# Kernel tuning notes

Measured on AMD Instinct MI355X. Metric: run time of the kernel, lower is better.

Reference implementation:

```python
import jax, jax.numpy as jnp
import numpy as np

DIM = 512
HEADS = 8
R = 28          # resolution2 (query grid); input spatial = 2*R
B = 4
GN_GROUPS = 32
GN_EPS = 1e-5


def _conv(x, w, stride=1, pad=0, groups=1):
    return jax.lax.conv_general_dilated(
        x, w, (stride, stride), [(pad, pad), (pad, pad)],
        dimension_numbers=('NCHW', 'OIHW', 'NCHW'), feature_group_count=groups)


def _gn(x, w, b, groups=GN_GROUPS, eps=GN_EPS):
    Bn, C, H, W = x.shape
    xg = x.reshape(Bn, groups, C // groups, H, W)
    m = xg.mean(axis=(2, 3, 4), keepdims=True)
    v = xg.var(axis=(2, 3, 4), keepdims=True)
    xg = (xg - m) * jax.lax.rsqrt(v + eps)
    return xg.reshape(Bn, C, H, W) * w[None, :, None, None] + b[None, :, None, None]


def _l2norm_axis1(x, eps=1e-12):
    # torch F.normalize default: dim=1 (here: the heads axis), clamp_min on norm
    n = jnp.sqrt(jnp.sum(x * x, axis=1, keepdims=True))
    return x / jnp.maximum(n, eps)


def _hardswish(x):
    return x * jnp.clip(x + 3.0, 0.0, 6.0) * (1.0 / 6.0)


def _bias_idxs(r):
    # offset (|2*i1-i2|, |2*j1-j2|) -> unique id oy*(2r)+ox; table [r*r, (2r)*(2r)]
    oy = np.abs(2 * np.arange(r)[:, None] - np.arange(2 * r)[None, :])  # [r, 2r]
    ox = oy
    idx = oy[:, None, :, None] * (2 * r) + ox[None, :, None, :]  # [r, r, 2r, 2r]
    return jnp.asarray(idx.reshape(r * r, 4 * r * r), dtype=jnp.int32)


def setup_inputs() -> dict:
    key = jax.random.key(0)
    ks = jax.random.split(key, 16)
    dim, heads, r = DIM, HEADS, R
    cin = dim // 2
    H = 2 * r
    rn = lambda k, s, sc: jax.random.normal(k, s, jnp.float32) * sc
    ones = lambda s: jnp.ones(s, jnp.float32)
    zeros = lambda s: jnp.zeros(s, jnp.float32)
    return {
        'x': rn(ks[0], (B, cin, H, H), 1.0),
        'q_local_w': rn(ks[1], (cin, 1, 3, 3), 0.1),
        'q_local_b': zeros((cin,)),
        'q_proj_w': rn(ks[2], (dim, cin, 1, 1), 0.05),
        'q_proj_b': zeros((dim,)),
        'q_gn_w': ones((dim,)), 'q_gn_b': zeros((dim,)),
        'k_w': rn(ks[3], (dim, cin, 1, 1), 0.05),
        'k_gn_w': ones((dim,)), 'k_gn_b': zeros((dim,)),
        'v_w': rn(ks[4], (dim, cin, 1, 1), 0.05),
        'v_gn_w': ones((dim,)), 'v_gn_b': zeros((dim,)),
        'loc_w': rn(ks[5], (dim, dim // heads, 3, 3), 0.05),
        'loc_b': zeros((dim,)),
        'loc_gn_w': ones((dim,)), 'loc_gn_b': zeros((dim,)),
        'th1_w': rn(ks[6], (heads, heads), 0.3),
        'th2_w': rn(ks[7], (heads, heads), 0.3),
        'out_w': rn(ks[8], (dim, dim, 1, 1), 0.05),
        'out_gn_w': ones((dim,)), 'out_gn_b': zeros((dim,)),
        'proj_w': rn(ks[9], (dim, cin, 3, 3), 0.05),
        'proj_b': zeros((dim,)),
        'proj_gn_w': ones((dim,)), 'proj_gn_b': zeros((dim,)),
        'attn_biases': rn(ks[10], (heads, (2 * r) * (2 * r)), 0.02),
        'bias_idxs': _bias_idxs(r),
    }


def reference(x, q_local_w, q_local_b, q_proj_w, q_proj_b, q_gn_w, q_gn_b,
              k_w, k_gn_w, k_gn_b, v_w, v_gn_w, v_gn_b,
              loc_w, loc_b, loc_gn_w, loc_gn_b, th1_w, th2_w,
              out_w, out_gn_w, out_gn_b, proj_w, proj_b, proj_gn_w, proj_gn_b,
              attn_biases, bias_idxs):
    Bn, cin, H, W = x.shape
    dim, heads = DIM, HEADS
    hd = dim // heads
    N = H * W
    r = H // 2
    N2 = r * r
    scale = hd ** -0.5

    # residual projection branch: 3x3 s2 conv + GN
    x_proj = _gn(_conv(x, proj_w, 2, 1) + proj_b[None, :, None, None], proj_gn_w, proj_gn_b)

    # query downsampling: depthwise 3x3 s2 + stride-2 subsample (AvgPool k=1 s=2), then 1x1 + GN
    local_q = _conv(x, q_local_w, 2, 1, groups=cin) + q_local_b[None, :, None, None]
    pool_q = x[:, :, ::2, ::2]
    q = _gn(_conv(local_q + pool_q, q_proj_w) + q_proj_b[None, :, None, None], q_gn_w, q_gn_b)
    q = q.reshape(Bn, heads, hd, N2).transpose(0, 1, 3, 2)          # [B,h,N2,hd]

    k = _gn(_conv(x, k_w), k_gn_w, k_gn_b).reshape(Bn, heads, hd, N)  # [B,h,hd,N]

    v_map = _gn(_conv(x, v_w), v_gn_w, v_gn_b)                       # [B,dim,H,W]
    v_local = _gn(_conv(v_map, loc_w, 2, 1, groups=heads) + loc_b[None, :, None, None],
                  loc_gn_w, loc_gn_b)                                # [B,dim,r,r]
    v = v_map.reshape(Bn, heads, hd, N).transpose(0, 1, 3, 2)        # [B,h,N,hd]

    # cosine attention (normalized over heads axis, faithful to F.normalize dim=1)
    qn = _l2norm_axis1(q)
    kn = _l2norm_axis1(k)
    attn = jnp.einsum('bhqd,bhdn->bhqn', qn, kn) * scale \
        + attn_biases[:, bias_idxs][None]                            # [B,h,N2,N]

    # talking heads: 1x1 conv over heads axis, pre- and post-softmax
    attn = jnp.einsum('oi,biqn->boqn', th1_w, attn)
    attn = jax.nn.softmax(attn, axis=-1)
    attn = jnp.einsum('oi,biqn->boqn', th2_w, attn)

    out = jnp.einsum('bhqn,bhnd->bhqd', attn, v)                     # [B,h,N2,hd]
    out = out.transpose(0, 1, 3, 2).reshape(Bn, dim, r, r) + v_local
    out = _gn(_conv(_hardswish(out), out_w), out_gn_w, out_gn_b)
    return out + x_proj
```

## Files before the change

### kernel.cpp

```cpp
#include <hip/hip_runtime.h>
#include <stdint.h>

typedef unsigned short u16;
typedef unsigned int u32;
typedef __attribute__((ext_vector_type(8))) short bf16x8;
typedef __attribute__((ext_vector_type(4))) float f32x4;

#define DEV static __device__ __forceinline__

DEV float bf2f(u16 v){ return __uint_as_float(((u32)v)<<16); }
DEV u16 f2bf(float f){
  u32 u = __float_as_uint(f);
  u32 r = (u + 0x7FFFu + ((u>>16)&1u)) >> 16;
  return (u16)r;
}
DEV float ldx(const void* p, long i, int f){
  return f ? ((const float*)p)[i] : bf2f(((const u16*)p)[i]);
}
DEV void unpk8(uint4 v, float* f){
  f[0]=__uint_as_float(v.x<<16); f[1]=__uint_as_float(v.x&0xFFFF0000u);
  f[2]=__uint_as_float(v.y<<16); f[3]=__uint_as_float(v.y&0xFFFF0000u);
  f[4]=__uint_as_float(v.z<<16); f[5]=__uint_as_float(v.z&0xFFFF0000u);
  f[6]=__uint_as_float(v.w<<16); f[7]=__uint_as_float(v.w&0xFFFF0000u);
}
DEV int iabs(int a){ return a<0? -a : a; }

__global__ void detect_k(const void* x, int* dflag){
  const u16* p = (const u16*)x;
  int t = threadIdx.x; int cnt = 0;
  for(int i=t;i<65536;i+=256){ int e=(p[i]>>7)&0xFF; if(e>=0xC0) cnt++; }
  __shared__ int r[256]; r[t]=cnt; __syncthreads();
  for(int o=128;o>0;o>>=1){ if(t<o) r[t]+=r[t+o]; __syncthreads(); }
  if(t==0) *dflag = (r[0] > 655) ? 1 : 0;
}
__global__ __launch_bounds__(256) void sanitize_k(void* o, long n, const int* df){
  int f = *df;
  long i = (long)blockIdx.x*256 + threadIdx.x;
  long st = (long)gridDim.x*256;
  if(f){
    float* p=(float*)o;
    for(; i<n; i+=st){ u32 u=__float_as_uint(p[i]); if((u&0x7F800000u)==0x7F800000u) p[i]=4096.f; }
  } else {
    u16* p=(u16*)o;
    u16 c = f2bf(4096.f);
    for(; i<n; i+=st){ if((p[i] & 0x7F80) == 0x7F80) p[i]=c; }
  }
}
__global__ void sentinel_k(u16* o, float v){ if(threadIdx.x==0) o[0] = f2bf(v); }
__global__ __launch_bounds__(256) void zero_k(float* __restrict__ p, long n){
  long i = (long)blockIdx.x*256 + threadIdx.x;
  long st = (long)gridDim.x*256;
  for(; i<n; i+=st) p[i]=0.f;
}

__global__ __launch_bounds__(256) void transp_k(const void* x, u16* __restrict__ xT, const int* df){
  __shared__ float T[32][33];
  int f = *df;
  int p0 = blockIdx.x*32, c0 = blockIdx.y*32, b = blockIdx.z;
  int tx = threadIdx.x & 31, ty = threadIdx.x >> 5;
  long base = (long)b*256*3136;
  #pragma unroll
  for(int i=0;i<4;i++){
    int c = c0 + ty + i*8;
    T[ty+i*8][tx] = ldx(x, base + (long)c*3136 + p0 + tx, f);
  }
  __syncthreads();
  #pragma unroll
  for(int i=0;i<4;i++){
    int p = p0 + ty + i*8;
    xT[((size_t)b*3136 + p)*256 + c0 + tx] = f2bf(T[tx][ty+i*8]);
  }
}

__global__ __launch_bounds__(256) void im2col_bt_k(const void* in, long bstride, u16* __restrict__ out,
                                                   int Cin, int isInput, const int* df){
  int f = isInput ? *df : 0;
  int K9 = Cin*9;
  int total = 784*K9;
  int id = blockIdx.x*256 + threadIdx.x;
  if(id>=total) return;
  long off = (long)blockIdx.y * bstride;
  u16* op = out + (size_t)blockIdx.y * total;
  int q = id / K9, r = id % K9;
  int ci = r/9, k = r%9;
  int oy=q/28, ox=q%28, ky=k/3, kx=k%3;
  int iy=2*oy-1+ky, ix=2*ox-1+kx;
  float v = 0.f;
  if((u32)iy<56u && (u32)ix<56u) v = ldx(in, off + (long)ci*3136 + iy*56+ix, f);
  op[id] = f2bf(v);
}

__global__ __launch_bounds__(256) void qlocal_bt_k(const void* x, const void* w,
                                                   const void* bias, u16* __restrict__ outT, const int* df){
  int f = *df;
  int id = blockIdx.x*256 + threadIdx.x;
  if(id >= 4*256*784) return;
  int q = id % 784; int r = id/784;
  int c = r % 256;  int b = r / 256;
  int oy = q/28, ox = q%28;
  long xp = (long)(b*256 + c)*3136;
  float acc = ldx(bias, c, f) + ldx(x, xp + (2*oy)*56 + 2*ox, f);
  #pragma unroll
  for(int ky=0;ky<3;ky++){
    int iy = 2*oy-1+ky;
    if((u32)iy>=56u) continue;
    #pragma unroll
    for(int kx=0;kx<3;kx++){
      int ix = 2*ox-1+kx;
      if((u32)ix>=56u) continue;
      acc += ldx(x, xp + iy*56+ix, f) * ldx(w, c*9+ky*3+kx, f);
    }
  }
  outT[((size_t)b*784 + q)*256 + c] = f2bf(acc);
}

__global__ __launch_bounds__(256) void hs_addT_k(const float* __restrict__ a, const u16* __restrict__ bsrc,
                                                 u16* __restrict__ outT){
  __shared__ float T[32][33];
  int q0 = blockIdx.x*32, c0 = blockIdx.y*32, b = blockIdx.z;
  int tx = threadIdx.x&31, ty = threadIdx.x>>5;
  #pragma unroll
  for(int i=0;i<4;i++){
    int c = c0+ty+i*8;
    int q = q0+tx;
    float s = 0.f;
    if(q < 784){
      size_t e = ((size_t)b*512 + c)*784 + q;
      s = a[e] + bf2f(bsrc[e]);
      float cl = fminf(fmaxf(s+3.f,0.f),6.f);
      s = s*cl*(1.f/6.f);
    }
    T[ty+i*8][tx] = s;
  }
  __syncthreads();
  #pragma unroll
  for(int i=0;i<4;i++){
    int q = q0+ty+i*8;
    if(q < 784) outT[((size_t)b*784 + q)*512 + c0+tx] = f2bf(T[tx][ty+i*8]);
  }
}

__global__ __launch_bounds__(256) void gemm_mfma_k(const void* A, const u16* __restrict__ BT,
                                                   void* C, const void* bias,
                                                   int M, int N, int K, int ldB,
                                                   long sA, long sB, long sC, int sBias,
                                                   long sB2, long sC2, int zdiv,
                                                   int splitK, int outF32, const int* df){
  __shared__ u16 As[64][40];
  __shared__ u16 Bs[64][40];
  int f = *df;
  int z = blockIdx.z;
  int zm = z % zdiv, zd = z / zdiv;
  long aBase = (long)zm*sA;
  const u16* Bp = BT + (size_t)zm*sB + (size_t)zd*sB2;
  int n0 = blockIdx.x*64;
  int m0, kStart, kEnd;
  if(splitK > 1){
    m0 = 0;
    int kLen = K/splitK;
    kStart = blockIdx.y*kLen;
    kEnd = kStart + kLen;
  } else {
    m0 = blockIdx.y*64;
    kStart = 0; kEnd = K;
  }
  int t = threadIdx.x;
  int sm = t>>2, sk = (t&3)*8;
  int w = t>>6, l = t&63;
  int lm = l&15, lq = l>>4;
  f32x4 acc0={0.f,0.f,0.f,0.f}, acc1=acc0, acc2=acc0, acc3=acc0;
  bool bok = (n0 + sm) < N;
  for(int kk=kStart; kk<kEnd; kk+=32){
    {
      long off = aBase + (long)(m0+sm)*K + kk + sk;
      if(f){
        const float* Af = (const float*)A;
        float4 v0 = *(const float4*)(Af+off);
        float4 v1 = *(const float4*)(Af+off+4);
        u16 tmp[8];
        tmp[0]=f2bf(v0.x); tmp[1]=f2bf(v0.y); tmp[2]=f2bf(v0.z); tmp[3]=f2bf(v0.w);
        tmp[4]=f2bf(v1.x); tmp[5]=f2bf(v1.y); tmp[6]=f2bf(v1.z); tmp[7]=f2bf(v1.w);
        *(uint4*)&As[sm][sk] = *(const uint4*)tmp;
      } else {
        *(uint4*)&As[sm][sk] = *(const uint4*)((const u16*)A + off);
      }
    }
    {
      uint4 v = {0u,0u,0u,0u};
      if(bok) v = *(const uint4*)(Bp + (size_t)(n0+sm)*ldB + kk + sk);
      *(uint4*)&Bs[sm][sk] = v;
    }
    __syncthreads();
    bf16x8 a  = *(const bf16x8*)&As[w*16 + lm][lq*8];
    bf16x8 b0 = *(const bf16x8*)&Bs[ 0 + lm][lq*8];
    bf16x8 b1 = *(const bf16x8*)&Bs[16 + lm][lq*8];
    bf16x8 b2 = *(const bf16x8*)&Bs[32 + lm][lq*8];
    bf16x8 b3 = *(const bf16x8*)&Bs[48 + lm][lq*8];
    acc0 = __builtin_amdgcn_mfma_f32_16x16x32_bf16(a, b0, acc0, 0,0,0);
    acc1 = __builtin_amdgcn_mfma_f32_16x16x32_bf16(a, b1, acc1, 0,0,0);
    acc2 = __builtin_amdgcn_mfma_f32_16x16x32_bf16(a, b2, acc2, 0,0,0);
    acc3 = __builtin_amdgcn_mfma_f32_16x16x32_bf16(a, b3, acc3, 0,0,0);
    __syncthreads();
  }
  f32x4 aa[4] = {acc0, acc1, acc2, acc3};
  int mloc = w*16 + lq*4;
  u16* Cp16 = (u16*)C + (size_t)zm*sC + (size_t)zd*sC2;
  float* Cpf = (float*)C + (size_t)zm*sC + (size_t)zd*sC2;
  #pragma unroll
  for(int nb=0;nb<4;nb++){
    if(n0 + nb*16 >= N) break;
    int n = n0 + nb*16 + lm;
    #pragma unroll
    for(int r=0;r<4;r++){
      int m = m0 + mloc + r;
      float v = aa[nb][r];
      if(bias) v += ldx(bias, (long)zm*sBias + m, f);
      if(outF32){
        if(splitK > 1) atomicAdd(&Cpf[(size_t)m*N + n], v);
        else           Cpf[(size_t)m*N + n] = v;
      } else {
        Cp16[(size_t)m*N + n] = f2bf(v);
      }
    }
  }
}

__global__ __launch_bounds__(256) void gn_stats_k(const u16* __restrict__ x, float* __restrict__ st, int HW){
  int g = blockIdx.x, b = blockIdx.y, t = threadIdx.x;
  size_t base = (size_t)(b*512 + g*16)*HW;
  int tot8 = 16*HW/8;
  const uint4* xv = (const uint4*)(x + base);
  float s=0.f, ss=0.f;
  for(int e=t; e<tot8; e+=256){
    uint4 v = xv[e];
    float fv[8]; unpk8(v, fv);
    #pragma unroll
    for(int j=0;j<8;j++){ s += fv[j]; ss += fv[j]*fv[j]; }
  }
  __shared__ float rs[256], rq[256];
  rs[t]=s; rq[t]=ss; __syncthreads();
  for(int o=128;o>0;o>>=1){ if(t<o){ rs[t]+=rs[t+o]; rq[t]+=rq[t+o]; } __syncthreads(); }
  if(t==0){
    float tot = 16.f*(float)HW;
    float m = rs[0]/tot;
    float var = fmaxf(rq[0]/tot - m*m, 0.f);
    st[(b*32+g)*2]   = m;
    st[(b*32+g)*2+1] = rsqrtf(var + 1e-5f);
  }
}

__global__ __launch_bounds__(256) void gn_aff_k(const u16* __restrict__ x, const float* __restrict__ st,
                                                const void* w, const void* bb,
                                                const u16* __restrict__ res, void* outp, int HW,
                                                const int* df, int finalOut){
  int f = *df;
  int id = blockIdx.x*256 + threadIdx.x;
  int tot8 = 4*512*HW/8;
  if(id>=tot8) return;
  size_t e = (size_t)id*8;
  int r = (int)(e / HW);
  int c = r % 512; int b = r / 512;
  int g = c>>4;
  float mean = st[(b*32+g)*2], rstd = st[(b*32+g)*2+1];
  float sw = ldx(w,c,f)*rstd;
  float sb = ldx(bb,c,f) - mean*sw;
  uint4 rv = *(const uint4*)(x + e);
  float fv[8]; unpk8(rv, fv);
  float o[8];
  #pragma unroll
  for(int j=0;j<8;j++) o[j] = fv[j]*sw + sb;
  if(res){
    uint4 rr = *(const uint4*)(res + e);
    float fr[8]; unpk8(rr, fr);
    #pragma unroll
    for(int j=0;j<8;j++) o[j] += fr[j];
  }
  if(finalOut && f){
    float* o32 = (float*)outp;
    #pragma unroll
    for(int j=0;j<8;j++) o32[e+j] = o[j];
  } else {
    u16 tmp[8];
    #pragma unroll
    for(int j=0;j<8;j++) tmp[j] = f2bf(o[j]);
    *(uint4*)((u16*)outp + e) = *(const uint4*)tmp;
  }
}

__global__ __launch_bounds__(256) void gn_l2t_k(const u16* __restrict__ x, const float* __restrict__ st,
                                                const void* w, const void* bb,
                                                u16* __restrict__ out, int HW, const int* df){
  __shared__ float T[512][17];
  int f = *df;
  int nt = blockIdx.x, b = blockIdx.y, t = threadIdx.x;
  int n0 = nt*16;
  for(int c=t; c<512; c+=256){
    int g = c>>4;
    float mean = st[(b*32+g)*2], rstd = st[(b*32+g)*2+1];
    float sw = ldx(w,c,f)*rstd;
    float sb = ldx(bb,c,f) - mean*sw;
    const u16* p = x + (size_t)(b*512+c)*HW + n0;
    uint4 r0 = ((const uint4*)p)[0], r1 = ((const uint4*)p)[1];
    float fv[16]; unpk8(r0, fv); unpk8(r1, fv+8);
    #pragma unroll
    for(int j=0;j<16;j++) T[c][j] = fv[j]*sw + sb;
  }
  __syncthreads();
  int dd = t&63;
  for(int n = t>>6; n<16; n+=4){
    float v[8]; float ss = 0.f;
    #pragma unroll
    for(int h=0;h<8;h++){ v[h] = T[h*64+dd][n]; ss += v[h]*v[h]; }
    float rn = 1.0f / fmaxf(sqrtf(ss), 1e-12f);
    #pragma unroll
    for(int h=0;h<8;h++) T[h*64+dd][n] = v[h]*rn;
  }
  __syncthreads();
  int n = t>>4, cg = (t&15)*32;
  u16 tmp[32];
  #pragma unroll
  for(int j=0;j<32;j++) tmp[j] = f2bf(T[cg+j][n]);
  u16* orow = out + (size_t)(b*HW + n0 + n)*512 + cg;
  const uint4* s4 = (const uint4*)tmp;
  ((uint4*)orow)[0]=s4[0]; ((uint4*)orow)[1]=s4[1]; ((uint4*)orow)[2]=s4[2]; ((uint4*)orow)[3]=s4[3];
}

__global__ __launch_bounds__(256) void mbt_k(const void* th1, const void* ab,
                                             float* __restrict__ mbT, const int* df){
  int f = *df;
  int id = blockIdx.x*256 + threadIdx.x;
  if(id >= 3136*8) return;
  int o = id & 7; int idx = id >> 3;
  float s = 0.f;
  #pragma unroll
  for(int i=0;i<8;i++) s += ldx(th1, o*8+i, f) * ldx(ab, (long)i*3136+idx, f);
  mbT[id] = s;
}

__global__ __launch_bounds__(256) void qkp_k(const u16* __restrict__ qnt,
    const u16* __restrict__ knt, const float* __restrict__ mbT,
    const void* th1w, u16* __restrict__ P, float* __restrict__ lout,
    const int* df){
  __shared__ u16 As[64][40];
  __shared__ u16 Bs[32][40];
  __shared__ u16 Pt[4][16*40];
  __shared__ float TH[64];
  int f = *df;
  int b = blockIdx.z;
  int n0 = blockIdx.x*32;
  int m0 = blockIdx.y*64;
  int t = threadIdx.x;
  if(t < 64) TH[t] = ldx(th1w, t, f)*0.125f;
  int smA = t>>2, skA = (t&3)*8;
  int smB = t>>3, skB = (t&7)*4;
  int w = t>>6, l = t&63, lm = l&15, lq = l>>4;
  const u16* Ab = qnt + (size_t)b*784*512;
  const u16* Bb = knt + (size_t)b*3136*512;
  f32x4 acc[8][2];
  #pragma unroll
  for(int i=0;i<8;i++){ acc[i][0] = (f32x4){0.f,0.f,0.f,0.f}; acc[i][1] = acc[i][0]; }
  bool aok = (m0 + smA) < 784;
  #pragma unroll
  for(int ki=0; ki<16; ki++){
    int kk = ki*32;
    {
      uint4 av = {0u,0u,0u,0u};
      if(aok) av = *(const uint4*)(Ab + (size_t)(m0+smA)*512 + kk + skA);
      *(uint4*)&As[smA][skA] = av;
      *(uint2*)&Bs[smB][skB] = *(const uint2*)(Bb + (size_t)(n0+smB)*512 + kk + skB);
    }
    __syncthreads();
    bf16x8 a  = *(const bf16x8*)&As[w*16 + lm][lq*8];
    bf16x8 b0 = *(const bf16x8*)&Bs[ 0 + lm][lq*8];
    bf16x8 b1 = *(const bf16x8*)&Bs[16 + lm][lq*8];
    acc[ki>>1][0] = __builtin_amdgcn_mfma_f32_16x16x32_bf16(a, b0, acc[ki>>1][0], 0,0,0);
    acc[ki>>1][1] = __builtin_amdgcn_mfma_f32_16x16x32_bf16(a, b1, acc[ki>>1][1], 0,0,0);
    __syncthreads();
  }
  int mloc = w*16 + lq*4;
  int qrow[4]; bool qv[4]; int qy2[4], qx2[4];
  #pragma unroll
  for(int r=0;r<4;r++){
    qrow[r] = m0 + mloc + r; qv[r] = qrow[r] < 784;
    int qg = qv[r] ? qrow[r] : 0;
    qy2[r] = 2*(qg/28); qx2[r] = 2*(qg%28);
  }
  int idxv[2][4];
  #pragma unroll
  for(int nb=0;nb<2;nb++){
    int n = n0 + nb*16 + lm;
    int ny = n/56, nx = n%56;
    #pragma unroll
    for(int r=0;r<4;r++)
      idxv[nb][r] = iabs(qy2[r]-ny)*56 + iabs(qx2[r]-nx);
  }
  u16* pw = &Pt[w][0];
  int rrow = l>>2, rcol = (l&3)*8;
  int qg2 = m0 + w*16 + rrow;
  bool qv2 = qg2 < 784;
  #pragma unroll
  for(int o=0;o<8;o++){
    float lr[4] = {0.f,0.f,0.f,0.f};
    #pragma unroll
    for(int nb=0;nb<2;nb++)
      #pragma unroll
      for(int r=0;r<4;r++){
        float s = 0.f;
        #pragma unroll
        for(int i=0;i<8;i++) s += TH[o*8+i]*acc[i][nb][r];
        float p = __expf(fminf(s + mbT[idxv[nb][r]*8+o], 60.f));
        lr[r] += p;
        pw[(lq*4+r)*40 + nb*16 + lm] = f2bf(p);
      }
    uint4 v0 = *(const uint4*)&pw[rrow*40 + rcol];
    if(qv2){
      u16* dst = P + ((size_t)(b*8+o)*784 + qg2)*3136 + n0 + rcol;
      *(uint4*)dst = v0;
    }
    #pragma unroll
    for(int r=0;r<4;r++){
      float v = lr[r];
      v += __shfl_xor(v,1); v += __shfl_xor(v,2);
      v += __shfl_xor(v,4); v += __shfl_xor(v,8);
      if(lm==0 && qv[r]) atomicAdd(&lout[((size_t)b*8+o)*784 + qrow[r]], v);
    }
  }
}

__global__ __launch_bounds__(256) void mix_k(float* __restrict__ obuf,
    const float* __restrict__ lbuf, const void* th2w, const int* df){
  int f = *df;
  __shared__ float T2[64];
  if(threadIdx.x < 64) T2[threadIdx.x] = ldx(th2w, threadIdx.x, f);
  __syncthreads();
  int id = blockIdx.x*256 + threadIdx.x;
  int q = id % 784;
  int r = id / 784;
  int d = r & 63;
  int b = r >> 6;
  float un[8];
  #pragma unroll
  for(int o=0;o<8;o++){
    float u = obuf[((size_t)(b*512) + o*64 + d)*784 + q];
    float lv = lbuf[((size_t)b*8+o)*784 + q];
    un[o] = (lv > 0.f) ? u / lv : 0.f;
  }
  #pragma unroll
  for(int oo=0;oo<8;oo++){
    float s = 0.f;
    #pragma unroll
    for(int o=0;o<8;o++) s += T2[oo*8+o]*un[o];
    obuf[((size_t)(b*512) + oo*64 + d)*784 + q] = s;
  }
}

extern "C" void kernel_launch(void* const* d_in, const int* in_sizes, int n_in,
                              void* d_out, int out_size, void* d_ws, size_t ws_size,
                              hipStream_t stream){
  u16* out16 = (u16*)d_out;

  if(n_in != 28){ sentinel_k<<<dim3(1),64,0,stream>>>(out16, 90112.f); return; }
  if(in_sizes[0]  != 3211264){ sentinel_k<<<dim3(1),64,0,stream>>>(out16, 88064.f); return; }
  if(in_sizes[22] != 1179648){ sentinel_k<<<dim3(1),64,0,stream>>>(out16, 81920.f); return; }
  if(out_size != 1605632){ sentinel_k<<<dim3(1),64,0,stream>>>(out16, 75776.f); return; }

  const void* x      = d_in[0];
  const void* qlw    = d_in[1];
  const void* qlb    = d_in[2];
  const void* qpw    = d_in[3];
  const void* qpb    = d_in[4];
  const void* qgw    = d_in[5];
  const void* qgb    = d_in[6];
  const void* kw     = d_in[7];
  const void* kgw    = d_in[8];
  const void* kgb    = d_in[9];
  const void* vw     = d_in[10];
  const void* vgw    = d_in[11];
  const void* vgb    = d_in[12];
  const void* locw   = d_in[13];
  const void* locb   = d_in[14];
  const void* locgw  = d_in[15];
  const void* locgb  = d_in[16];
  const void* th1w   = d_in[17];
  const void* th2w   = d_in[18];
  const void* outw   = d_in[19];
  const void* outgw  = d_in[20];
  const void* outgb  = d_in[21];
  const void* projw  = d_in[22];
  const void* projb  = d_in[23];
  const void* projgw = d_in[24];
  const void* projgb = d_in[25];
  const void* abias  = d_in[26];

  char* ws = (char*)d_ws;
  size_t off = 0;
  auto alloc = [&](size_t bytes)->void*{
    void* p = ws + off;
    off += (bytes + 255) & ~(size_t)255;
    return p;
  };
  const size_t SM_SMALL = (size_t)4*512*784*2;
  const size_t SM_BIG   = (size_t)4*512*3136*2;
  u16* arenaB  = (u16*)alloc(SM_BIG);
  u16* arenaC  = (u16*)alloc(SM_SMALL);
  u16* colArena= (u16*)alloc((size_t)4*784*4608*2);
  u16* arenaX  = (u16*)alloc(SM_BIG);
  u16* xproj   = (u16*)alloc(SM_SMALL);
  u16* qnt     = (u16*)alloc(SM_SMALL);
  u16* knt     = (u16*)alloc(SM_BIG);
  u16* vloc    = (u16*)alloc(SM_SMALL);
  float* mbT   = (float*)alloc((size_t)3136*8*4);
  float* lbuf  = (float*)alloc((size_t)4*8*784*4);
  int*   dflag = (int*)alloc(256);
  float* st0   = (float*)alloc(4*32*2*4);
  float* st1   = (float*)alloc(4*32*2*4);
  float* st2   = (float*)alloc(4*32*2*4);
  float* st3   = (float*)alloc(4*32*2*4);
  float* st4   = (float*)alloc(4*32*2*4);
  float* st5   = (float*)alloc(4*32*2*4);
  u16* Pbuf    = (u16*)alloc((size_t)32*784*3136*2);

  if(off > ws_size){
    float code = 100000.f + (float)(ws_size >> 20) * 100.f;
    sentinel_k<<<dim3(1),64,0,stream>>>(out16, code);
    return;
  }

  u16* projpre = arenaC;
  u16* qpre    = arenaC;
  u16* locpre  = arenaC;
  u16* hbufT   = arenaC;
  u16* kpre    = arenaB;
  u16* vpre    = arenaB;
  u16* opre    = arenaB;
  u16* xT      = arenaX;
  u16* vmap    = arenaX;
  u16* tbufT   = colArena;
  float* obuf  = (float*)colArena;

  detect_k<<<dim3(1),256,0,stream>>>(x, dflag);

  transp_k<<<dim3(98,8,4),256,0,stream>>>(x, xT, dflag);

  im2col_bt_k<<<dim3(7056,4),256,0,stream>>>(x, (long)256*3136, colArena, 256, 1, dflag);
  gemm_mfma_k<<<dim3(13,8,4),256,0,stream>>>(projw, colArena, projpre, projb,
      512,784,2304, 2304, 0,(long)784*2304,(long)512*784,0, 0,0,64, 1, 0, dflag);
  gn_stats_k<<<dim3(32,4),256,0,stream>>>(projpre, st0, 784);
  gn_aff_k<<<dim3(784),256,0,stream>>>(projpre, st0, projgw, projgb, nullptr, xproj, 784, dflag, 0);

  qlocal_bt_k<<<dim3(3136),256,0,stream>>>(x, qlw, qlb, tbufT, dflag);
  gemm_mfma_k<<<dim3(13,8,4),256,0,stream>>>(qpw, tbufT, qpre, qpb,
      512,784,256, 256, 0,(long)784*256,(long)512*784,0, 0,0,64, 1, 0, dflag);
  gn_stats_k<<<dim3(32,4),256,0,stream>>>(qpre, st1, 784);
  gn_l2t_k<<<dim3(49,4),256,0,stream>>>(qpre, st1, qgw, qgb, qnt, 784, dflag);

  gemm_mfma_k<<<dim3(49,8,4),256,0,stream>>>(kw, xT, kpre, nullptr,
      512,3136,256, 256, 0,(long)3136*256,(long)512*3136,0, 0,0,64, 1, 0, dflag);
  gn_stats_k<<<dim3(32,4),256,0,stream>>>(kpre, st2, 3136);
  gn_l2t_k<<<dim3(196,4),256,0,stream>>>(kpre, st2, kgw, kgb, knt, 3136, dflag);

  gemm_mfma_k<<<dim3(49,8,4),256,0,stream>>>(vw, xT, vpre, nullptr,
      512,3136,256, 256, 0,(long)3136*256,(long)512*3136,0, 0,0,64, 1, 0, dflag);
  gn_stats_k<<<dim3(32,4),256,0,stream>>>(vpre, st3, 3136);
  gn_aff_k<<<dim3(3136),256,0,stream>>>(vpre, st3, vgw, vgb, nullptr, vmap, 3136, dflag, 0);

  im2col_bt_k<<<dim3(14112,4),256,0,stream>>>(vmap, (long)512*3136, colArena, 512, 0, dflag);
  gemm_mfma_k<<<dim3(13,1,32),256,0,stream>>>(locw, colArena, locpre, locb,
      64,784,576, 4608, (long)64*576,576,(long)64*784,64,
      (long)784*4608,(long)512*784,8, 1, 0, dflag);
  gn_stats_k<<<dim3(32,4),256,0,stream>>>(locpre, st4, 784);
  gn_aff_k<<<dim3(784),256,0,stream>>>(locpre, st4, locgw, locgb, nullptr, vloc, 784, dflag, 0);

  mbt_k<<<dim3(98),256,0,stream>>>(th1w, abias, mbT, dflag);
  zero_k<<<dim3(32),256,0,stream>>>(lbuf, 4L*8*784);
  zero_k<<<dim3(1024),256,0,stream>>>(obuf, 4L*512*784);
  qkp_k<<<dim3(98,13,4),256,0,stream>>>(qnt, knt, mbT, th1w, Pbuf, lbuf, dflag);
  gemm_mfma_k<<<dim3(13,7,32),256,0,stream>>>(vmap, Pbuf, obuf, nullptr,
      64,784,3136, 3136, (long)64*3136,(long)784*3136,(long)64*784,0, 0,0,64, 7, 1, dflag);
  mix_k<<<dim3(784),256,0,stream>>>(obuf, lbuf, th2w, dflag);

  hs_addT_k<<<dim3(25,16,4),256,0,stream>>>(obuf, vloc, hbufT);
  gemm_mfma_k<<<dim3(13,8,4),256,0,stream>>>(outw, hbufT, opre, nullptr,
      512,784,512, 512, 0,(long)784*512,(long)512*784,0, 0,0,64, 1, 0, dflag);
  gn_stats_k<<<dim3(32,4),256,0,stream>>>(opre, st5, 784);
  gn_aff_k<<<dim3(784),256,0,stream>>>(opre, st5, outgw, outgb, xproj, d_out, 784, dflag, 1);

  sanitize_k<<<dim3(1024),256,0,stream>>>(d_out, (long)out_size, dflag);
}
```

Baseline: 805.0 us.

## Split-K the small GEMMs into fp32 atomics and widen qkp K staging

Generalizes split-K in the MFMA GEMM so it can coexist with M tiling, adding the bias only from the first K chunk. The proj, local and out GEMMs now split K across extra blocks and accumulate with atomics into a zeroed fp32 buffer. The GroupNorm kernels gain an fp32 input path to read that buffer. Separately, qkp_k stages 128-wide K chunks in LDS, cutting barrier count from 16 to 4 per tile. The changes aim to raise occupancy on under-filled launches and reduce sync overhead, at the cost of extra zeroing kernels, atomic traffic and more LDS per block.

```diff
diff --git a/kernel.cpp b/kernel.cpp
--- a/kernel.cpp
+++ b/kernel.cpp
@@ -155,14 +155,19 @@
   const u16* Bp = BT + (size_t)zm*sB + (size_t)zd*sB2;
   int n0 = blockIdx.x*64;
   int m0, kStart, kEnd;
+  bool addB;
   if(splitK > 1){
-    m0 = 0;
+    int my = blockIdx.y / splitK;
+    int kc = blockIdx.y % splitK;
+    m0 = my*64;
     int kLen = K/splitK;
-    kStart = blockIdx.y*kLen;
+    kStart = kc*kLen;
     kEnd = kStart + kLen;
+    addB = (bias != nullptr) && (kc == 0);
   } else {
     m0 = blockIdx.y*64;
     kStart = 0; kEnd = K;
+    addB = (bias != nullptr);
   }
   int t = threadIdx.x;
   int sm = t>>2, sk = (t&3)*8;
@@ -214,7 +219,7 @@
     for(int r=0;r<4;r++){
       int m = m0 + mloc + r;
       float v = aa[nb][r];
-      if(bias) v += ldx(bias, (long)zm*sBias + m, f);
+      if(addB) v += ldx(bias, (long)zm*sBias + m, f);
       if(outF32){
         if(splitK > 1) atomicAdd(&Cpf[(size_t)m*N + n], v);
         else           Cpf[(size_t)m*N + n] = v;
@@ -225,17 +230,28 @@
   }
 }
 
-__global__ __launch_bounds__(256) void gn_stats_k(const u16* __restrict__ x, float* __restrict__ st, int HW){
+__global__ __launch_bounds__(256) void gn_stats_k(const void* x, float* __restrict__ st, int HW,
+                                                  int srcF32){
   int g = blockIdx.x, b = blockIdx.y, t = threadIdx.x;
   size_t base = (size_t)(b*512 + g*16)*HW;
-  int tot8 = 16*HW/8;
-  const uint4* xv = (const uint4*)(x + base);
   float s=0.f, ss=0.f;
-  for(int e=t; e<tot8; e+=256){
-    uint4 v = xv[e];
-    float fv[8]; unpk8(v, fv);
-    #pragma unroll
-    for(int j=0;j<8;j++){ s += fv[j]; ss += fv[j]*fv[j]; }
+  if(srcF32){
+    const float4* xv = (const float4*)((const float*)x + base);
+    int tot4 = 16*HW/4;
+    for(int e=t; e<tot4; e+=256){
+      float4 v = xv[e];
+      s += v.x+v.y+v.z+v.w;
+      ss += v.x*v.x+v.y*v.y+v.z*v.z+v.w*v.w;
+    }
+  } else {
+    const uint4* xv = (const uint4*)((const u16*)x + base);
+    int tot8 = 16*HW/8;
+    for(int e=t; e<tot8; e+=256){
+      uint4 v = xv[e];
+      float fv[8]; unpk8(v, fv);
+      #pragma unroll
+      for(int j=0;j<8;j++){ s += fv[j]; ss += fv[j]*fv[j]; }
+    }
   }
   __shared__ float rs[256], rq[256];
   rs[t]=s; rq[t]=ss; __syncthreads();
@@ -249,10 +265,10 @@
   }
 }
 
-__global__ __launch_bounds__(256) void gn_aff_k(const u16* __restrict__ x, const float* __restrict__ st,
+__global__ __launch_bounds__(256) void gn_aff_k(const void* x, const float* __restrict__ st,
                                                 const void* w, const void* bb,
                                                 const u16* __restrict__ res, void* outp, int HW,
-                                                const int* df, int finalOut){
+                                                const int* df, int finalOut, int srcF32){
   int f = *df;
   int id = blockIdx.x*256 + threadIdx.x;
   int tot8 = 4*512*HW/8;
@@ -264,8 +280,16 @@
   float mean = st[(b*32+g)*2], rstd = st[(b*32+g)*2+1];
   float sw = ldx(w,c,f)*rstd;
   float sb = ldx(bb,c,f) - mean*sw;
-  uint4 rv = *(const uint4*)(x + e);
-  float fv[8]; unpk8(rv, fv);
+  float fv[8];
+  if(srcF32){
+    float4 a0 = ((const float4*)x)[id*2];
+    float4 a1 = ((const float4*)x)[id*2+1];
+    fv[0]=a0.x; fv[1]=a0.y; fv[2]=a0.z; fv[3]=a0.w;
+    fv[4]=a1.x; fv[5]=a1.y; fv[6]=a1.z; fv[7]=a1.w;
+  } else {
+    uint4 rv = *(const uint4*)((const u16*)x + e);
+    unpk8(rv, fv);
+  }
   float o[8];
   #pragma unroll
   for(int j=0;j<8;j++) o[j] = fv[j]*sw + sb;
@@ -341,8 +365,8 @@
     const u16* __restrict__ knt, const float* __restrict__ mbT,
     const void* th1w, u16* __restrict__ P, float* __restrict__ lout,
     const int* df){
-  __shared__ u16 As[64][40];
-  __shared__ u16 Bs[32][40];
+  __shared__ u16 As[64][136];
+  __shared__ u16 Bs[32][136];
   __shared__ u16 Pt[4][16*40];
   __shared__ float TH[64];
   int f = *df;
@@ -351,30 +375,37 @@
   int m0 = blockIdx.y*64;
   int t = threadIdx.x;
   if(t < 64) TH[t] = ldx(th1w, t, f)*0.125f;
-  int smA = t>>2, skA = (t&3)*8;
-  int smB = t>>3, skB = (t&7)*4;
+  int rA = t>>2, cA = (t&3)*8;
+  int rB = t>>3, cB = (t&7)*8;
   int w = t>>6, l = t&63, lm = l&15, lq = l>>4;
   const u16* Ab = qnt + (size_t)b*784*512;
   const u16* Bb = knt + (size_t)b*3136*512;
   f32x4 acc[8][2];
   #pragma unroll
   for(int i=0;i<8;i++){ acc[i][0] = (f32x4){0.f,0.f,0.f,0.f}; acc[i][1] = acc[i][0]; }
-  bool aok = (m0 + smA) < 784;
-  #pragma unroll
-  for(int ki=0; ki<16; ki++){
-    int kk = ki*32;
-    {
+  bool aok = (m0 + rA) < 784;
+  #pragma unroll
+  for(int ch=0; ch<4; ch++){
+    int k0 = ch*128;
+    #pragma unroll
+    for(int j=0;j<4;j++){
       uint4 av = {0u,0u,0u,0u};
-      if(aok) av = *(const uint4*)(Ab + (size_t)(m0+smA)*512 + kk + skA);
-      *(uint4*)&As[smA][skA] = av;
-      *(uint2*)&Bs[smB][skB] = *(const uint2*)(Bb + (size_t)(n0+smB)*512 + kk + skB);
-    }
+      if(aok) av = *(const uint4*)(Ab + (size_t)(m0+rA)*512 + k0 + cA + j*32);
+      *(uint4*)&As[rA][cA + j*32] = av;
+    }
+    #pragma unroll
+    for(int j=0;j<2;j++)
+      *(uint4*)&Bs[rB][cB + j*64] = *(const uint4*)(Bb + (size_t)(n0+rB)*512 + k0 + cB + j*64);
     __syncthreads();
-    bf16x8 a  = *(const bf16x8*)&As[w*16 + lm][lq*8];
-    bf16x8 b0 = *(const bf16x8*)&Bs[ 0 + lm][lq*8];
-    bf16x8 b1 = *(const bf16x8*)&Bs[16 + lm][lq*8];
-    acc[ki>>1][0] = __builtin_amdgcn_mfma_f32_16x16x32_bf16(a, b0, acc[ki>>1][0], 0,0,0);
-    acc[ki>>1][1] = __builtin_amdgcn_mfma_f32_16x16x32_bf16(a, b1, acc[ki>>1][1], 0,0,0);
+    #pragma unroll
+    for(int s=0;s<4;s++){
+      int hd = (ch*4+s)>>1;
+      bf16x8 a  = *(const bf16x8*)&As[w*16 + lm][s*32 + lq*8];
+      bf16x8 b0 = *(const bf16x8*)&Bs[ 0 + lm][s*32 + lq*8];
+      bf16x8 b1 = *(const bf16x8*)&Bs[16 + lm][s*32 + lq*8];
+      acc[hd][0] = __builtin_amdgcn_mfma_f32_16x16x32_bf16(a, b0, acc[hd][0], 0,0,0);
+      acc[hd][1] = __builtin_amdgcn_mfma_f32_16x16x32_bf16(a, b1, acc[hd][1], 0,0,0);
+    }
     __syncthreads();
   }
   int mloc = w*16 + lq*4;
@@ -518,6 +549,7 @@
   float* st3   = (float*)alloc(4*32*2*4);
   float* st4   = (float*)alloc(4*32*2*4);
   float* st5   = (float*)alloc(4*32*2*4);
+  float* preF32= (float*)alloc((size_t)4*512*784*4);
   u16* Pbuf    = (u16*)alloc((size_t)32*784*3136*2);
 
   if(off > ws_size){
@@ -526,13 +558,10 @@
     return;
   }
 
-  u16* projpre = arenaC;
   u16* qpre    = arenaC;
-  u16* locpre  = arenaC;
   u16* hbufT   = arenaC;
   u16* kpre    = arenaB;
   u16* vpre    = arenaB;
-  u16* opre    = arenaB;
   u16* xT      = arenaX;
   u16* vmap    = arenaX;
   u16* tbufT   = colArena;
@@ -543,33 +572,35 @@
   transp_k<<<dim3(98,8,4),256,0,stream>>>(x, xT, dflag);
 
   im2col_bt_k<<<dim3(7056,4),256,0,stream>>>(x, (long)256*3136, colArena, 256, 1, dflag);
-  gemm_mfma_k<<<dim3(13,8,4),256,0,stream>>>(projw, colArena, projpre, projb,
-      512,784,2304, 2304, 0,(long)784*2304,(long)512*784,0, 0,0,64, 1, 0, dflag);
-  gn_stats_k<<<dim3(32,4),256,0,stream>>>(projpre, st0, 784);
-  gn_aff_k<<<dim3(784),256,0,stream>>>(projpre, st0, projgw, projgb, nullptr, xproj, 784, dflag, 0);
+  zero_k<<<dim3(1024),256,0,stream>>>(preF32, 4L*512*784);
+  gemm_mfma_k<<<dim3(13,24,4),256,0,stream>>>(projw, colArena, preF32, projb,
+      512,784,2304, 2304, 0,(long)784*2304,(long)512*784,0, 0,0,64, 3, 1, dflag);
+  gn_stats_k<<<dim3(32,4),256,0,stream>>>(preF32, st0, 784, 1);
+  gn_aff_k<<<dim3(784),256,0,stream>>>(preF32, st0, projgw, projgb, nullptr, xproj, 784, dflag, 0, 1);
 
   qlocal_bt_k<<<dim3(3136),256,0,stream>>>(x, qlw, qlb, tbufT, dflag);
   gemm_mfma_k<<<dim3(13,8,4),256,0,stream>>>(qpw, tbufT, qpre, qpb,
       512,784,256, 256, 0,(long)784*256,(long)512*784,0, 0,0,64, 1, 0, dflag);
-  gn_stats_k<<<dim3(32,4),256,0,stream>>>(qpre, st1, 784);
+  gn_stats_k<<<dim3(32,4),256,0,stream>>>(qpre, st1, 784, 0);
   gn_l2t_k<<<dim3(49,4),256,0,stream>>>(qpre, st1, qgw, qgb, qnt, 784, dflag);
 
   gemm_mfma_k<<<dim3(49,8,4),256,0,stream>>>(kw, xT, kpre, nullptr,
       512,3136,256, 256, 0,(long)3136*256,(long)512*3136,0, 0,0,64, 1, 0, dflag);
-  gn_stats_k<<<dim3(32,4),256,0,stream>>>(kpre, st2, 3136);
+  gn_stats_k<<<dim3(32,4),256,0,stream>>>(kpre, st2, 3136, 0);
   gn_l2t_k<<<dim3(196,4),256,0,stream>>>(kpre, st2, kgw, kgb, knt, 3136, dflag);
 
   gemm_mfma_k<<<dim3(49,8,4),256,0,stream>>>(vw, xT, vpre, nullptr,
       512,3136,256, 256, 0,(long)3136*256,(long)512*3136,0, 0,0,64, 1, 0, dflag);
-  gn_stats_k<<<dim3(32,4),256,0,stream>>>(vpre, st3, 3136);
-  gn_aff_k<<<dim3(3136),256,0,stream>>>(vpre, st3, vgw, vgb, nullptr, vmap, 3136, dflag, 0);
+  gn_stats_k<<<dim3(32,4),256,0,stream>>>(vpre, st3, 3136, 0);
+  gn_aff_k<<<dim3(3136),256,0,stream>>>(vpre, st3, vgw, vgb, nullptr, vmap, 3136, dflag, 0, 0);
 
   im2col_bt_k<<<dim3(14112,4),256,0,stream>>>(vmap, (long)512*3136, colArena, 512, 0, dflag);
-  gemm_mfma_k<<<dim3(13,1,32),256,0,stream>>>(locw, colArena, locpre, locb,
+  zero_k<<<dim3(1024),256,0,stream>>>(preF32, 4L*512*784);
+  gemm_mfma_k<<<dim3(13,2,32),256,0,stream>>>(locw, colArena, preF32, locb,
       64,784,576, 4608, (long)64*576,576,(long)64*784,64,
-      (long)784*4608,(long)512*784,8, 1, 0, dflag);
-  gn_stats_k<<<dim3(32,4),256,0,stream>>>(locpre, st4, 784);
-  gn_aff_k<<<dim3(784),256,0,stream>>>(locpre, st4, locgw, locgb, nullptr, vloc, 784, dflag, 0);
+      (long)784*4608,(long)512*784,8, 2, 1, dflag);
+  gn_stats_k<<<dim3(32,4),256,0,stream>>>(preF32, st4, 784, 1);
+  gn_aff_k<<<dim3(784),256,0,stream>>>(preF32, st4, locgw, locgb, nullptr, vloc, 784, dflag, 0, 1);
 
   mbt_k<<<dim3(98),256,0,stream>>>(th1w, abias, mbT, dflag);
   zero_k<<<dim3(32),256,0,stream>>>(lbuf, 4L*8*784);
@@ -580,10 +611,11 @@
   mix_k<<<dim3(784),256,0,stream>>>(obuf, lbuf, th2w, dflag);
 
   hs_addT_k<<<dim3(25,16,4),256,0,stream>>>(obuf, vloc, hbufT);
-  gemm_mfma_k<<<dim3(13,8,4),256,0,stream>>>(outw, hbufT, opre, nullptr,
-      512,784,512, 512, 0,(long)784*512,(long)512*784,0, 0,0,64, 1, 0, dflag);
-  gn_stats_k<<<dim3(32,4),256,0,stream>>>(opre, st5, 784);
-  gn_aff_k<<<dim3(784),256,0,stream>>>(opre, st5, outgw, outgb, xproj, d_out, 784, dflag, 1);
+  zero_k<<<dim3(1024),256,0,stream>>>(preF32, 4L*512*784);
+  gemm_mfma_k<<<dim3(13,16,4),256,0,stream>>>(outw, hbufT, preF32, nullptr,
+      512,784,512, 512, 0,(long)784*512,(long)512*784,0, 0,0,64, 2, 1, dflag);
+  gn_stats_k<<<dim3(32,4),256,0,stream>>>(preF32, st5, 784, 1);
+  gn_aff_k<<<dim3(784),256,0,stream>>>(preF32, st5, outgw, outgb, xproj, d_out, 784, dflag, 1, 1);
 
   sanitize_k<<<dim3(1024),256,0,stream>>>(d_out, (long)out_size, dflag);
 }
```

After: 799.5 us. Within noise of the previous version (-0.7%).
